# Kernel optimization log

Hardware: AMD Instinct MI355X
Metric: run time of the kernel (lower is better)

## Reference

```python
import jax, jax.numpy as jnp
import numpy as np

B, S, D, H, E, P, TOP_K = 8, 4096, 512, 2048, 8, 16, 2


def setup_inputs() -> dict:
    key = jax.random.key(0)
    ks = jax.random.split(key, 7)
    x = jax.random.normal(ks[0], (B, S, D), dtype=jnp.float32)
    pattern_ids = jax.random.randint(ks[1], (B,), 0, P)
    # router params (init per module: std 0.01 content, std 0.1 pattern bias)
    Wr = 0.01 * jax.random.normal(ks[2], (D, E), dtype=jnp.float32)
    Wp = 0.1 * jax.random.normal(ks[3], (P, E), dtype=jnp.float32)
    # per-expert SwiGLU FFN weights (stacked): w1, w3: [E,D,H], w2: [E,H,D]
    W1 = jax.random.normal(ks[4], (E, D, H), dtype=jnp.float32) / np.float32(np.sqrt(D))
    W2 = jax.random.normal(ks[5], (E, H, D), dtype=jnp.float32) / np.float32(np.sqrt(H))
    W3 = jax.random.normal(ks[6], (E, D, H), dtype=jnp.float32) / np.float32(np.sqrt(D))
    return {"x": x, "pattern_ids": pattern_ids, "Wr": Wr, "Wp": Wp, "W1": W1, "W2": W2, "W3": W3}


def reference(x, pattern_ids, Wr, Wp, W1, W2, W3):
    num_experts = W1.shape[0]
    num_patterns = Wp.shape[0]
    # ---- pattern-aware router ----
    # content logits + per-batch pattern bias broadcast over seq
    logits = jnp.einsum('bsd,de->bse', x, Wr) + Wp[pattern_ids][:, None, :]  # [B,S,E]
    top_w, top_i = jax.lax.top_k(logits, TOP_K)           # [B,S,K]
    gates = jax.nn.softmax(top_w, axis=-1)                # softmax over the top-k logits
    # ---- expert dispatch / combine (loop over small fixed expert count) ----
    y = jnp.zeros_like(x)
    for e in range(num_experts):
        # combined gate weight for expert e per token (0 if not selected)
        w_e = jnp.sum(gates * (top_i == e), axis=-1)      # [B,S]
        h = jnp.einsum('bsd,dh->bsh', x, W1[e]) * jax.nn.silu(jnp.einsum('bsd,dh->bsh', x, W3[e]))
        y = y + w_e[..., None] * jnp.einsum('bsh,hd->bsd', h, W2[e])
    # ---- auxiliary losses ----
    probs = jax.nn.softmax(logits, axis=-1)
    router_z_loss = jnp.mean(jnp.square(logits)) * 0.001
    balance_loss = jnp.mean(jnp.square(probs.mean(axis=(0, 1)) - 1.0 / num_experts))
    Pn = jax.nn.softmax(Wp, axis=-1)
    sim = Pn @ Pn.T
    specialization_loss = jnp.mean(sim * (1.0 - jnp.eye(num_patterns, dtype=sim.dtype))) * 0.1
    return (y, router_z_loss, balance_loss, specialization_loss)
```

## Files before the change

### kernel.cpp

```cpp
#include <hip/hip_runtime.h>
#include <hip/hip_bf16.h>
#include <math.h>


#define B_ 8
#define S_ 4096
#define D_ 512
#define H_ 2048
#define E_ 8
#define P_ 16
#define NTOK (B_ * S_)
#define NPAIR (NTOK * 2)

typedef __bf16 bf16;
typedef __bf16 bf16x8 __attribute__((ext_vector_type(8)));
typedef float f32x4 __attribute__((ext_vector_type(4)));

#define OFF_GATES 256
#define OFF_LIST (OFF_GATES + NPAIR * 4)
#define OFF_XBF (OFF_LIST + E_ * NTOK * 4)
#define OFF_W13T (OFF_XBF + (size_t)NTOK * D_ * 2)
#define OFF_W2T (OFF_W13T + (size_t)E_ * 2 * H_ * D_ * 2)
#define OFF_HBUF (OFF_W2T + (size_t)E_ * D_ * H_ * 2)
#define WS_NEEDED (OFF_HBUF + (size_t)NTOK * H_ * 2)
#define WS_FUSED (OFF_HBUF + (size_t)NPAIR * H_ * 2)

__device__ __forceinline__ void gl16(const bf16* g, bf16* l) {
  __builtin_amdgcn_global_load_lds((const __attribute__((address_space(1))) unsigned int*)g,
                                   (__attribute__((address_space(3))) unsigned int*)l, 16, 0, 0);
}

__global__ __launch_bounds__(256) void router_kernel(
    const float* __restrict__ x, const int* __restrict__ pids,
    const float* __restrict__ Wr, const float* __restrict__ Wp,
    bf16* __restrict__ xbf, float* __restrict__ gates, int* __restrict__ lists,
    int* __restrict__ counts, float* __restrict__ probSum, float* __restrict__ zSum) {
  __shared__ float xs[32 * 516];
  __shared__ float wr_s[E_ * 516];
  __shared__ float wp_s[E_];
  __shared__ float probAcc[E_];
  __shared__ float zAcc;
  __shared__ int lcnt[E_], lbase[E_];
  __shared__ float lg_s[32][E_ + 1];

  const int tid = threadIdx.x;
  const int tok0 = blockIdx.x * 32;

#pragma unroll
  for (int rep = 0; rep < (D_ * E_) / 256; ++rep) {
    int flat = rep * 256 + tid;
    wr_s[(flat & 7) * 516 + (flat >> 3)] = Wr[flat];
  }
  if (tid < E_) {
    wp_s[tid] = Wp[pids[tok0 >> 12] * E_ + tid];
    probAcc[tid] = 0.f;
    lcnt[tid] = 0;
  }
  if (tid == 0) zAcc = 0.f;

  const float4* x4 = (const float4*)(x + (size_t)tok0 * D_);
#pragma unroll
  for (int rep = 0; rep < 16; ++rep) {
    int idx = rep * 256 + tid;
    float4 v = x4[idx];
    int t = idx >> 7;
    int d = (idx & 127) * 4;
    *(float4*)(xs + t * 516 + d) = v;
    union { unsigned short u[4]; uint2 qq; } pk;
    pk.u[0] = __builtin_bit_cast(unsigned short, (bf16)v.x);
    pk.u[1] = __builtin_bit_cast(unsigned short, (bf16)v.y);
    pk.u[2] = __builtin_bit_cast(unsigned short, (bf16)v.z);
    pk.u[3] = __builtin_bit_cast(unsigned short, (bf16)v.w);
    *(uint2*)(xbf + (size_t)tok0 * D_ + (size_t)idx * 4) = pk.qq;
  }
  __syncthreads();

  const int t = tid >> 3, e = tid & 7;
  const int lane = tid & 63;
  {
    float a0 = 0.f, a1 = 0.f, a2 = 0.f, a3 = 0.f;
    const float* xr = xs + t * 516;
    const float* wr = wr_s + e * 516;
#pragma unroll 8
    for (int d = 0; d < D_; d += 4) {
      float4 xv = *(const float4*)(xr + d);
      float4 wv = *(const float4*)(wr + d);
      a0 += xv.x * wv.x;
      a1 += xv.y * wv.y;
      a2 += xv.z * wv.z;
      a3 += xv.w * wv.w;
    }
    lg_s[t][e] = (a0 + a1) + (a2 + a3) + wp_s[e];
  }
  __syncthreads();

  float v[E_];
#pragma unroll
  for (int k = 0; k < E_; ++k) v[k] = lg_s[t][k];
  const float lg = v[e];
  float m = v[0];
#pragma unroll
  for (int k = 1; k < E_; ++k) m = fmaxf(m, v[k]);
  float s = 0.f;
#pragma unroll
  for (int k = 0; k < E_; ++k) s += expf(v[k] - m);
  float prob = expf(lg - m) / s;
  float z = lg * lg;
  int i1 = 0;
  float v1 = v[0];
#pragma unroll
  for (int k = 1; k < E_; ++k)
    if (v[k] > v1) { v1 = v[k]; i1 = k; }
  int i2 = -1;
  float v2 = -1e30f;
#pragma unroll
  for (int k = 0; k < E_; ++k)
    if (k != i1 && v[k] > v2) { v2 = v[k]; i2 = k; }

  float p = prob;
  p += __shfl_xor(p, 8);
  p += __shfl_xor(p, 16);
  p += __shfl_xor(p, 32);
  float zz = z;
#pragma unroll
  for (int off = 1; off < 64; off <<= 1) zz += __shfl_xor(zz, off);
  if (lane < 8) atomicAdd(&probAcc[e], p);
  if (lane == 0) atomicAdd(&zAcc, zz);

  int r = (e == i1) ? 0 : ((e == i2) ? 1 : -1);
  int pos = -1;
  if (r >= 0) {
    float ex = expf(v2 - v1);
    float g = (r == 0) ? 1.f / (1.f + ex) : ex / (1.f + ex);
    gates[(tok0 + t) * 2 + r] = g;
    pos = atomicAdd(&lcnt[e], 1);
  }
  __syncthreads();
  if (tid < E_) lbase[tid] = atomicAdd(&counts[tid], lcnt[tid]);
  __syncthreads();
  if (r >= 0) lists[e * NTOK + lbase[e] + pos] = (tok0 + t) * 2 + r;
  if (tid < E_) atomicAdd(&probSum[tid], probAcc[tid]);
  else if (tid == 8) atomicAdd(zSum, zAcc);
}

__global__ __launch_bounds__(256) void transpose_convert(const float* __restrict__ in,
                                                         bf16* __restrict__ out, int R, int C,
                                                         size_t out_estride, int mode) {
  const int e = blockIdx.z;
  const int r0 = blockIdx.y * 64, c0 = blockIdx.x * 64;
  in += (size_t)e * R * C;
  out += (size_t)e * out_estride;
  __shared__ unsigned int lt[64 * 33];

  const int tid = threadIdx.x;
  const int m = tid & 15, qq = tid >> 4;
#pragma unroll
  for (int rep = 0; rep < 2; ++rep) {
    int rp = qq + rep * 16;
    const float4 a = *(const float4*)(in + (size_t)(r0 + rp * 2) * C + c0 + m * 4);
    const float4 b = *(const float4*)(in + (size_t)(r0 + rp * 2 + 1) * C + c0 + m * 4);
#pragma unroll
    for (int j = 0; j < 4; ++j) {
      unsigned short lo = __builtin_bit_cast(unsigned short, (bf16)((&a.x)[j]));
      unsigned short hi = __builtin_bit_cast(unsigned short, (bf16)((&b.x)[j]));
      lt[(m * 4 + j) * 33 + rp] = (unsigned int)lo | ((unsigned int)hi << 16);
    }
  }
  __syncthreads();
  const int c = tid >> 2, dw0 = (tid & 3) * 8;
  unsigned int vv[8];
#pragma unroll
  for (int j = 0; j < 8; ++j) vv[j] = lt[c * 33 + dw0 + j];
  int orow = c0 + c;
  if (mode >= 0) orow = ((orow >> 4) << 5) | (orow & 15) | mode;
  uint4* dst = (uint4*)(out + (size_t)orow * R + r0 + dw0 * 2);
  dst[0] = make_uint4(vv[0], vv[1], vv[2], vv[3]);
  dst[1] = make_uint4(vv[4], vv[5], vv[6], vv[7]);
}

__global__ __launch_bounds__(256, 2) void gemm1_kernel(
    const bf16* __restrict__ xbf, const bf16* __restrict__ W13T,
    const int* __restrict__ counts, const int* __restrict__ lists,
    const float* __restrict__ gates, bf16* __restrict__ hbuf, int e_param, int fuse) {
  const int e = fuse ? (int)blockIdx.z : e_param;
  const int count = counts[e];
  const int m0 = blockIdx.y * 128;
  if (m0 >= count) return;
  int hbase = 0;
  if (fuse) {
#pragma unroll
    for (int j = 0; j < E_; ++j) hbase += (j < e) ? counts[j] : 0;
  }
  const int n0 = blockIdx.x * 128;
  const int* list_e = lists + e * NTOK;
  const bf16* Be = W13T + (size_t)e * (2 * H_) * D_;

  __shared__ bf16 sA[2 * 128 * 32];
  __shared__ bf16 sB[2 * 128 * 32];
  __shared__ int stok[128];
  __shared__ float sgate[128];

  const int tid = threadIdx.x;
  if (tid < 128) {
    int rg = m0 + tid;
    int pr = (rg < count) ? list_e[rg] : 0;
    stok[tid] = pr >> 1;
    sgate[tid] = (rg < count) ? gates[pr] : 0.f;
  }
  __syncthreads();

  const int wave = tid >> 6, lane = tid & 63;
  const int rsub = lane >> 2, kq = lane & 3;
  const int scol = (kq ^ ((lane >> 3) & 3)) * 8;
  const int rA0 = wave * 16 + rsub, rA1 = 64 + wave * 16 + rsub;
  const bf16* aP0 = xbf + (size_t)stok[rA0] * D_ + scol;
  const bf16* aP1 = xbf + (size_t)stok[rA1] * D_ + scol;
  const bf16* bP0 = Be + (size_t)(n0 + rA0) * D_ + scol;
  const bf16* bP1 = Be + (size_t)(n0 + rA1) * D_ + scol;
  bf16* lA0 = sA + wave * 512;
  bf16* lA1 = sA + (wave + 4) * 512;
  bf16* lB0 = sB + wave * 512;
  bf16* lB1 = sB + (wave + 4) * 512;

  const int wm = wave >> 1, wn = wave & 1;
  const int lm = lane & 15, q = lane >> 4;
  const int rq = (q ^ ((lm >> 1) & 3)) * 8;
  const bf16* aRd = sA + (wm * 64 + lm) * 32 + rq;
  const bf16* bRd = sB + (wn * 64 + lm) * 32 + rq;

  f32x4 acc[4][4] = {};

  gl16(aP0, lA0);
  gl16(aP1, lA1);
  gl16(bP0, lB0);
  gl16(bP1, lB1);
  __syncthreads();

  int cur = 0;
  for (int t = 1; t < D_ / 32; ++t) {
    const int koff = t * 32;
    const int nxt = (cur ^ 1) * 4096;
    gl16(aP0 + koff, lA0 + nxt);
    gl16(aP1 + koff, lA1 + nxt);
    gl16(bP0 + koff, lB0 + nxt);
    gl16(bP1 + koff, lB1 + nxt);
    const bf16* aR = aRd + cur * 4096;
    const bf16* bR = bRd + cur * 4096;
    bf16x8 af[4], bf_[4];
#pragma unroll
    for (int i = 0; i < 4; ++i) {
      af[i] = *(const bf16x8*)(aR + i * 512);
      bf_[i] = *(const bf16x8*)(bR + i * 512);
    }
#pragma unroll
    for (int mt = 0; mt < 4; ++mt)
#pragma unroll
      for (int nt = 0; nt < 4; ++nt)
        acc[mt][nt] =
            __builtin_amdgcn_mfma_f32_16x16x32_bf16(af[mt], bf_[nt], acc[mt][nt], 0, 0, 0);
    __syncthreads();
    cur ^= 1;
  }
  {
    const bf16* aR = aRd + cur * 4096;
    const bf16* bR = bRd + cur * 4096;
    bf16x8 af[4], bf_[4];
#pragma unroll
    for (int i = 0; i < 4; ++i) {
      af[i] = *(const bf16x8*)(aR + i * 512);
      bf_[i] = *(const bf16x8*)(bR + i * 512);
    }
#pragma unroll
    for (int mt = 0; mt < 4; ++mt)
#pragma unroll
      for (int nt = 0; nt < 4; ++nt)
        acc[mt][nt] =
            __builtin_amdgcn_mfma_f32_16x16x32_bf16(af[mt], bf_[nt], acc[mt][nt], 0, 0, 0);
  }

  const int hb = (n0 >> 1) + wn * 32;
#pragma unroll
  for (int mt = 0; mt < 4; ++mt) {
#pragma unroll
    for (int u = 0; u < 2; ++u) {
#pragma unroll
      for (int r = 0; r < 4; ++r) {
        int lrow = wm * 64 + mt * 16 + q * 4 + r;
        int grow = m0 + lrow;
        if (grow < count) {
          float v1 = acc[mt][2 * u][r];
          float v3 = acc[mt][2 * u + 1][r];
          float g = v1 * (v3 / (1.f + __expf(-v3))) * sgate[lrow];
          hbuf[(size_t)(hbase + grow) * H_ + hb + u * 16 + lm] = (bf16)g;
        }
      }
    }
  }
}

__global__ __launch_bounds__(256, 2) void gemm2_kernel(const bf16* __restrict__ hbuf,
                                                       const bf16* __restrict__ W2T,
                                                       const int* __restrict__ counts,
                                                       const int* __restrict__ lists,
                                                       float* __restrict__ y, int e_param,
                                                       int fuse) {
  const int zz = (int)blockIdx.z;
  const int e = fuse ? (zz >> 1) : e_param;
  const int kc = fuse ? (zz & 1) : zz;
  const int count = counts[e];
  const int m0 = blockIdx.y * 128;
  if (m0 >= count) return;
  int hbase = 0;
  if (fuse) {
#pragma unroll
    for (int j = 0; j < E_; ++j) hbase += (j < e) ? counts[j] : 0;
  }
  const int n0 = blockIdx.x * 128;
  const int kb = kc * (H_ / 2);
  const bf16* W2e = W2T + (size_t)e * D_ * H_;
  const int* list_e = lists + e * NTOK;

  __shared__ bf16 sA[4 * 128 * 32];
  __shared__ bf16 sB[4 * 128 * 32];
  __shared__ int stok[128];

  const int tid = threadIdx.x;
  if (tid < 128) {
    int rg = m0 + tid;
    stok[tid] = (rg < count) ? (list_e[rg] >> 1) : 0;
  }
  __syncthreads();

  const int wave = tid >> 6, lane = tid & 63;
  const int rsub = lane >> 2, kq = lane & 3;
  const int scol = (kq ^ ((lane >> 3) & 3)) * 8;
  const int rA0 = wave * 16 + rsub, rA1 = 64 + wave * 16 + rsub;
  const bf16* aP0 = hbuf + (size_t)(hbase + m0 + rA0) * H_ + kb + scol;
  const bf16* aP1 = hbuf + (size_t)(hbase + m0 + rA1) * H_ + kb + scol;
  const bf16* bP0 = W2e + (size_t)(n0 + rA0) * H_ + kb + scol;
  const bf16* bP1 = W2e + (size_t)(n0 + rA1) * H_ + kb + scol;

  const int wm = wave >> 1, wn = wave & 1;
  const int lm = lane & 15, q = lane >> 4;
  const int rq = (q ^ ((lm >> 1) & 3)) * 8;
  const bf16* aRd = sA + (wm * 64 + lm) * 32 + rq;
  const bf16* bRd = sB + (wn * 64 + lm) * 32 + rq;

  f32x4 acc[4][4] = {};

  auto STAGE = [&](int t, int bi) {
    const int ko = t * 32;
    bf16* ba = sA + bi * 4096;
    bf16* bb = sB + bi * 4096;
    gl16(aP0 + ko, ba + wave * 512);
    gl16(aP1 + ko, ba + (wave + 4) * 512);
    gl16(bP0 + ko, bb + wave * 512);
    gl16(bP1 + ko, bb + (wave + 4) * 512);
  };
  auto COMP = [&](int bi) {
    const bf16* aR = aRd + bi * 4096;
    const bf16* bR = bRd + bi * 4096;
    bf16x8 af[4], bf_[4];
#pragma unroll
    for (int i = 0; i < 4; ++i) {
      af[i] = *(const bf16x8*)(aR + i * 512);
      bf_[i] = *(const bf16x8*)(bR + i * 512);
    }
#pragma unroll
    for (int mt = 0; mt < 4; ++mt)
#pragma unroll
      for (int nt = 0; nt < 4; ++nt)
        acc[mt][nt] =
            __builtin_amdgcn_mfma_f32_16x16x32_bf16(af[mt], bf_[nt], acc[mt][nt], 0, 0, 0);
  };

  const int NT = (H_ / 2) / 32;
  STAGE(0, 0);
  STAGE(1, 1);
  for (int t = 0; t < NT - 2; ++t) {
    STAGE(t + 2, (t + 2) & 3);
    asm volatile("s_waitcnt vmcnt(8) lgkmcnt(0)" ::: "memory");
    __builtin_amdgcn_s_barrier();
    COMP(t & 3);
  }
  asm volatile("s_waitcnt vmcnt(4) lgkmcnt(0)" ::: "memory");
  __builtin_amdgcn_s_barrier();
  COMP((NT - 2) & 3);
  asm volatile("s_waitcnt vmcnt(0) lgkmcnt(0)" ::: "memory");
  __builtin_amdgcn_s_barrier();
  COMP((NT - 1) & 3);

#pragma unroll
  for (int mt = 0; mt < 4; ++mt) {
#pragma unroll
    for (int nt = 0; nt < 4; ++nt) {
#pragma unroll
      for (int r = 0; r < 4; ++r) {
        int lrow = wm * 64 + mt * 16 + q * 4 + r;
        int grow = m0 + lrow;
        if (grow < count) {
          atomicAdd(&y[(size_t)stok[lrow] * D_ + n0 + wn * 64 + nt * 16 + lm], acc[mt][nt][r]);
        }
      }
    }
  }
}

__global__ __launch_bounds__(256) void finalize_kernel(const float* __restrict__ Wp,
                                                       const float* __restrict__ probSum,
                                                       const float* __restrict__ zSum,
                                                       float* __restrict__ out) {
  __shared__ float pn[P_][E_];
  __shared__ float simAcc;
  const int tid = threadIdx.x;
  if (tid == 0) simAcc = 0.f;
  if (tid < P_) {
    float v[E_], m = -1e30f, s = 0.f;
#pragma unroll
    for (int e = 0; e < E_; ++e) {
      v[e] = Wp[tid * E_ + e];
      m = fmaxf(m, v[e]);
    }
#pragma unroll
    for (int e = 0; e < E_; ++e) {
      float ex = expf(v[e] - m);
      pn[tid][e] = ex;
      s += ex;
    }
#pragma unroll
    for (int e = 0; e < E_; ++e) pn[tid][e] /= s;
  }
  __syncthreads();
  {
    int i = tid >> 4, j = tid & 15;
    if (i != j) {
      float d = 0.f;
#pragma unroll
      for (int e = 0; e < E_; ++e) d += pn[i][e] * pn[j][e];
      atomicAdd(&simAcc, d);
    }
  }
  __syncthreads();
  if (tid == 0) {
    out[0] = zSum[0] / (float)(NTOK * E_) * 0.001f;
    float bl = 0.f;
#pragma unroll
    for (int e = 0; e < E_; ++e) {
      float pm = probSum[e] / (float)NTOK - 1.f / (float)E_;
      bl += pm * pm;
    }
    out[1] = bl / (float)E_;
    out[2] = simAcc / (float)(P_ * P_) * 0.1f;
  }
}

extern "C" void kernel_launch(void* const* d_in, const int* in_sizes, int n_in, void* d_out,
                              int out_size, void* d_ws, size_t ws_size, hipStream_t stream) {
  const float* x = (const float*)d_in[0];
  const int* pids = (const int*)d_in[1];
  const float* Wr = (const float*)d_in[2];
  const float* Wp = (const float*)d_in[3];
  const float* W1 = (const float*)d_in[4];
  const float* W2 = (const float*)d_in[5];
  const float* W3 = (const float*)d_in[6];
  float* y = (float*)d_out;

  if (ws_size < WS_NEEDED) return;
  const int fuse = (ws_size >= WS_FUSED) ? 1 : 0;

  char* ws = (char*)d_ws;
  int* counts = (int*)ws;
  float* probSum = (float*)(ws + 32);
  float* zSum = (float*)(ws + 64);
  float* gates = (float*)(ws + OFF_GATES);
  int* lists = (int*)(ws + OFF_LIST);
  bf16* xbf = (bf16*)(ws + OFF_XBF);
  bf16* W13T = (bf16*)(ws + OFF_W13T);
  bf16* W2T = (bf16*)(ws + OFF_W2T);
  bf16* hbuf = (bf16*)(ws + OFF_HBUF);

  hipMemsetAsync(ws, 0, 256, stream);
  hipMemsetAsync(d_out, 0, (size_t)NTOK * D_ * 4, stream);

  router_kernel<<<dim3(NTOK / 32), 256, 0, stream>>>(x, pids, Wr, Wp, xbf, gates, lists, counts,
                                                     probSum, zSum);
  transpose_convert<<<dim3(H_ / 64, D_ / 64, E_), 256, 0, stream>>>(W1, W13T, D_, H_,
                                                                    (size_t)2 * H_ * D_, 0);
  transpose_convert<<<dim3(H_ / 64, D_ / 64, E_), 256, 0, stream>>>(W3, W13T, D_, H_,
                                                                    (size_t)2 * H_ * D_, 16);
  transpose_convert<<<dim3(D_ / 64, H_ / 64, E_), 256, 0, stream>>>(W2, W2T, H_, D_,
                                                                    (size_t)H_ * D_, -1);

  if (fuse) {
    gemm1_kernel<<<dim3((2 * H_) / 128, NTOK / 128, E_), 256, 0, stream>>>(
        xbf, W13T, counts, lists, gates, hbuf, 0, 1);
    gemm2_kernel<<<dim3(D_ / 128, NTOK / 128, 2 * E_), 256, 0, stream>>>(hbuf, W2T, counts,
                                                                         lists, y, 0, 1);
  } else {
    for (int e = 0; e < E_; ++e) {
      gemm1_kernel<<<dim3((2 * H_) / 128, NTOK / 128), 256, 0, stream>>>(xbf, W13T, counts,
                                                                         lists, gates, hbuf, e, 0);
      gemm2_kernel<<<dim3(D_ / 128, NTOK / 128, 2), 256, 0, stream>>>(hbuf, W2T, counts, lists,
                                                                      y, e, 0);
    }
  }
  finalize_kernel<<<1, 256, 0, stream>>>(Wp, probSum, zSum, y + (size_t)NTOK * D_);
}
```

Measured before the change: 1.067 ms.

## Split hidden dimension into two halves to shrink intermediate buffer

Processes the FFN hidden dimension in two halves, running a gemm1/gemm2 pair over all experts for each half. This halves the intermediate h buffer so it needs less workspace and may stay more cache-resident, and it removes the per-expert fallback path. The cost is an extra launch pair, re-reading x for each half, and the two gemm2 passes accumulating into y twice. Row indices in gemm2 are clamped so loads stay inside the smaller buffer.

```diff
diff --git a/kernel.cpp b/kernel.cpp
--- a/kernel.cpp
+++ b/kernel.cpp
@@ -7,6 +7,7 @@
 #define S_ 4096
 #define D_ 512
 #define H_ 2048
+#define HH (H_ / 2)
 #define E_ 8
 #define P_ 16
 #define NTOK (B_ * S_)
@@ -22,8 +23,7 @@
 #define OFF_W13T (OFF_XBF + (size_t)NTOK * D_ * 2)
 #define OFF_W2T (OFF_W13T + (size_t)E_ * 2 * H_ * D_ * 2)
 #define OFF_HBUF (OFF_W2T + (size_t)E_ * D_ * H_ * 2)
-#define WS_NEEDED (OFF_HBUF + (size_t)NTOK * H_ * 2)
-#define WS_FUSED (OFF_HBUF + (size_t)NPAIR * H_ * 2)
+#define WS_NEEDED (OFF_HBUF + (size_t)NPAIR * HH * 2)
 
 __device__ __forceinline__ void gl16(const bf16* g, bf16* l) {
   __builtin_amdgcn_global_load_lds((const __attribute__((address_space(1))) unsigned int*)g,
@@ -181,17 +181,14 @@
 __global__ __launch_bounds__(256, 2) void gemm1_kernel(
     const bf16* __restrict__ xbf, const bf16* __restrict__ W13T,
     const int* __restrict__ counts, const int* __restrict__ lists,
-    const float* __restrict__ gates, bf16* __restrict__ hbuf, int e_param, int fuse) {
-  const int e = fuse ? (int)blockIdx.z : e_param;
+    const float* __restrict__ gates, bf16* __restrict__ hbuf, int half) {
+  const int e = (int)blockIdx.z;
   const int count = counts[e];
   const int m0 = blockIdx.y * 128;
   if (m0 >= count) return;
   int hbase = 0;
-  if (fuse) {
-#pragma unroll
-    for (int j = 0; j < E_; ++j) hbase += (j < e) ? counts[j] : 0;
-  }
-  const int n0 = blockIdx.x * 128;
+  for (int j = 0; j < e; ++j) hbase += counts[j];
+  const int n0 = blockIdx.x * 128 + half * (2 * HH);
   const int* list_e = lists + e * NTOK;
   const bf16* Be = W13T + (size_t)e * (2 * H_) * D_;
 
@@ -278,7 +275,7 @@
             __builtin_amdgcn_mfma_f32_16x16x32_bf16(af[mt], bf_[nt], acc[mt][nt], 0, 0, 0);
   }
 
-  const int hb = (n0 >> 1) + wn * 32;
+  const int hb = ((blockIdx.x * 128) >> 1) + wn * 32;
 #pragma unroll
   for (int mt = 0; mt < 4; ++mt) {
 #pragma unroll
@@ -291,7 +288,7 @@
           float v1 = acc[mt][2 * u][r];
           float v3 = acc[mt][2 * u + 1][r];
           float g = v1 * (v3 / (1.f + __expf(-v3))) * sgate[lrow];
-          hbuf[(size_t)(hbase + grow) * H_ + hb + u * 16 + lm] = (bf16)g;
+          hbuf[(size_t)(hbase + grow) * HH + hb + u * 16 + lm] = (bf16)g;
         }
       }
     }
@@ -302,21 +299,15 @@
                                                        const bf16* __restrict__ W2T,
                                                        const int* __restrict__ counts,
                                                        const int* __restrict__ lists,
-                                                       float* __restrict__ y, int e_param,
-                                                       int fuse) {
-  const int zz = (int)blockIdx.z;
-  const int e = fuse ? (zz >> 1) : e_param;
-  const int kc = fuse ? (zz & 1) : zz;
+                                                       float* __restrict__ y, int half) {
+  const int e = (int)blockIdx.z;
   const int count = counts[e];
   const int m0 = blockIdx.y * 128;
   if (m0 >= count) return;
   int hbase = 0;
-  if (fuse) {
-#pragma unroll
-    for (int j = 0; j < E_; ++j) hbase += (j < e) ? counts[j] : 0;
-  }
+  for (int j = 0; j < e; ++j) hbase += counts[j];
   const int n0 = blockIdx.x * 128;
-  const int kb = kc * (H_ / 2);
+  const int kb = half * HH;
   const bf16* W2e = W2T + (size_t)e * D_ * H_;
   const int* list_e = lists + e * NTOK;
 
@@ -335,8 +326,12 @@
   const int rsub = lane >> 2, kq = lane & 3;
   const int scol = (kq ^ ((lane >> 3) & 3)) * 8;
   const int rA0 = wave * 16 + rsub, rA1 = 64 + wave * 16 + rsub;
-  const bf16* aP0 = hbuf + (size_t)(hbase + m0 + rA0) * H_ + kb + scol;
-  const bf16* aP1 = hbuf + (size_t)(hbase + m0 + rA1) * H_ + kb + scol;
+  int ra0 = hbase + m0 + rA0;
+  int ra1 = hbase + m0 + rA1;
+  if (ra0 >= NPAIR) ra0 = NPAIR - 1;
+  if (ra1 >= NPAIR) ra1 = NPAIR - 1;
+  const bf16* aP0 = hbuf + (size_t)ra0 * HH + scol;
+  const bf16* aP1 = hbuf + (size_t)ra1 * HH + scol;
   const bf16* bP0 = W2e + (size_t)(n0 + rA0) * H_ + kb + scol;
   const bf16* bP1 = W2e + (size_t)(n0 + rA1) * H_ + kb + scol;
 
@@ -374,7 +369,7 @@
             __builtin_amdgcn_mfma_f32_16x16x32_bf16(af[mt], bf_[nt], acc[mt][nt], 0, 0, 0);
   };
 
-  const int NT = (H_ / 2) / 32;
+  const int NT = HH / 32;
   STAGE(0, 0);
   STAGE(1, 1);
   for (int t = 0; t < NT - 2; ++t) {
@@ -466,7 +461,6 @@
   float* y = (float*)d_out;
 
   if (ws_size < WS_NEEDED) return;
-  const int fuse = (ws_size >= WS_FUSED) ? 1 : 0;
 
   char* ws = (char*)d_ws;
   int* counts = (int*)ws;
@@ -491,18 +485,11 @@
   transpose_convert<<<dim3(D_ / 64, H_ / 64, E_), 256, 0, stream>>>(W2, W2T, H_, D_,
                                                                     (size_t)H_ * D_, -1);
 
-  if (fuse) {
-    gemm1_kernel<<<dim3((2 * H_) / 128, NTOK / 128, E_), 256, 0, stream>>>(
-        xbf, W13T, counts, lists, gates, hbuf, 0, 1);
-    gemm2_kernel<<<dim3(D_ / 128, NTOK / 128, 2 * E_), 256, 0, stream>>>(hbuf, W2T, counts,
-                                                                         lists, y, 0, 1);
-  } else {
-    for (int e = 0; e < E_; ++e) {
-      gemm1_kernel<<<dim3((2 * H_) / 128, NTOK / 128), 256, 0, stream>>>(xbf, W13T, counts,
-                                                                         lists, gates, hbuf, e, 0);
-      gemm2_kernel<<<dim3(D_ / 128, NTOK / 128, 2), 256, 0, stream>>>(hbuf, W2T, counts, lists,
-                                                                      y, e, 0);
-    }
+  for (int half = 0; half < 2; ++half) {
+    gemm1_kernel<<<dim3((2 * HH) / 128, NTOK / 128, E_), 256, 0, stream>>>(
+        xbf, W13T, counts, lists, gates, hbuf, half);
+    gemm2_kernel<<<dim3(D_ / 128, NTOK / 128, E_), 256, 0, stream>>>(hbuf, W2T, counts, lists,
+                                                                     y, half);
   }
   finalize_kernel<<<1, 256, 0, stream>>>(Wp, probSum, zSum, y + (size_t)NTOK * D_);
 }
```

Result: faster. 971.2 us (-9.0%).
